# Performance work log

Measured on AMD Instinct MI355X. Metric: run time of the kernel, lower is better.

Reference implementation:

```python
import jax, jax.numpy as jnp
import numpy as np

NUM_PRODUCT = 100000
NUM_USERS = 10000
EMBED_DIM = 512
H = EMBED_DIM // 2          # gru_hidden_size = embedding_dim // 2
MBS = 20                    # max_basket_size
NB = 64                     # baskets per user
K = 256                     # batch of users
B = NB * MBS                # flattened item positions per user
L = 2                       # GRU layers


def setup_inputs() -> dict:
    key = jax.random.key(0)
    ks = jax.random.split(key, 8)
    filter_basket_prob = jax.random.uniform(ks[0], (K, B), dtype=jnp.float32)
    # item ids in [-1, NUM_PRODUCT-1]; -1 is padding (shifted to padding_idx 0)
    input_seq_tensor = jax.random.randint(ks[1], (K, B), 0, NUM_PRODUCT + 1) - 1
    uid = jax.random.randint(ks[2], (K,), 0, NUM_USERS)
    embed_table = 0.02 * jax.random.normal(ks[3], (NUM_PRODUCT + 1, H), dtype=jnp.float32)
    embed_table = embed_table.at[0].set(0.0)  # padding_idx=0
    s = 1.0 / np.sqrt(H)
    w_ih = jax.random.uniform(ks[4], (L, 3 * H, H), jnp.float32, -s, s)
    w_hh = jax.random.uniform(ks[5], (L, 3 * H, H), jnp.float32, -s, s)
    b_ih = jax.random.uniform(ks[6], (L, 3 * H), jnp.float32, -s, s)
    b_hh = jax.random.uniform(ks[7], (L, 3 * H), jnp.float32, -s, s)
    return {"filter_basket_prob": filter_basket_prob, "input_seq_tensor": input_seq_tensor,
            "uid": uid, "embed_table": embed_table,
            "w_ih": w_ih, "w_hh": w_hh, "b_ih": b_ih, "b_hh": b_hh}


def _gru_layer(x, wih, whh, bih, bhh):
    # x: [K, T, H]; torch GRU gate math (r, z, n gate order)
    gi = jnp.einsum('kth,gh->ktg', x, wih) + bih  # [K, T, 3H]

    def step(h, gi_t):
        gh = h @ whh.T + bhh
        ir, iz, inn = jnp.split(gi_t, 3, axis=-1)
        hr, hz, hn = jnp.split(gh, 3, axis=-1)
        r = jax.nn.sigmoid(ir + hr)
        z = jax.nn.sigmoid(iz + hz)
        n = jnp.tanh(inn + r * hn)
        h_new = (1.0 - z) * n + z * h
        return h_new, h_new

    h0 = jnp.zeros((x.shape[0], whh.shape[1]), x.dtype)
    _, hs = jax.lax.scan(step, h0, jnp.swapaxes(gi, 0, 1))  # [T, K, H]
    return jnp.swapaxes(hs, 0, 1)


def reference(filter_basket_prob, input_seq_tensor, uid, embed_table, w_ih, w_hh, b_ih, b_hh):
    Kb, Bb = filter_basket_prob.shape
    Hh = embed_table.shape[1]
    nb = Bb // MBS
    # mask out padding positions (constant w.r.t. grads, as in torch .detach())
    mask = (input_seq_tensor != -1).astype(jnp.float32)
    prob = filter_basket_prob * mask                      # [K, B]
    emb = embed_table[input_seq_tensor + 1]               # [K, B, H]
    emb_f = (emb * prob[..., None]).reshape(Kb, nb, MBS, Hh)
    prob_b = prob.reshape(Kb, nb, MBS)
    filter_b = prob_b.max(axis=-1)                        # [K, NB]
    # avg basket pooling: sum(prob*emb) / (sum(prob) + eps)
    basket_emb = emb_f.sum(axis=2) / (prob_b.sum(axis=-1, keepdims=True) + 1e-10)
    valid = (filter_b > 0).astype(jnp.int32)
    # stable descending sort moves valid baskets to the front, preserving order
    order = jnp.argsort(-valid, axis=-1)                  # [K, NB]
    lengths = valid.sum(axis=-1)
    lengths = lengths + (lengths == 0).astype(lengths.dtype)  # clamp to >= 1
    x = jnp.take_along_axis(basket_emb, order[:, :, None], axis=1)  # [K, NB, H]
    # pack/pad/unsort in the original cancel out: GRU output at t depends only
    # on inputs <= t, so run the full padded scan and read step lengths-1.
    for l in range(w_ih.shape[0]):
        x = _gru_layer(x, w_ih[l], w_hh[l], b_ih[l], b_hh[l])
    return x[jnp.arange(Kb), lengths - 1]                 # [K, H]
```

## Files before the change

### kernel.cpp

```cpp
#include <hip/hip_runtime.h>
#include <cstdint>

#define KU 256
#define NBASK 64
#define MBS 20
#define BITEMS 1280
#define HD 256
#define G3 768
#define TT 64

typedef short v8s __attribute__((ext_vector_type(8)));
typedef float v4f __attribute__((ext_vector_type(4)));
typedef unsigned short v4us __attribute__((ext_vector_type(4)));
typedef unsigned int v4u __attribute__((ext_vector_type(4)));

__device__ __forceinline__ unsigned short f2b(float f){
  uint32_t u = __float_as_uint(f);
  u += 0x7FFFu + ((u >> 16) & 1u);
  return (unsigned short)(u >> 16);
}
__device__ __forceinline__ float b2f(unsigned short s){
  return __uint_as_float(((uint32_t)s) << 16);
}
__device__ __forceinline__ unsigned int packf(float x){
  unsigned short hi = f2b(x);
  unsigned short lo = f2b(x - b2f(hi));
  return ((unsigned int)hi << 16) | lo;
}
__device__ __forceinline__ float unpackf(unsigned int v){
  return b2f((unsigned short)(v >> 16)) + b2f((unsigned short)(v & 0xffffu));
}
__device__ __forceinline__ void waitflag(int* f, int v){
  while (__hip_atomic_load(f, __ATOMIC_ACQUIRE, __HIP_MEMORY_SCOPE_AGENT) < v)
    __builtin_amdgcn_s_sleep(2);
}

__global__ __launch_bounds__(1024) void k_convert(
    const float* __restrict__ wih, const float* __restrict__ whh,
    unsigned short* __restrict__ wih1hi, unsigned short* __restrict__ wih1lo,
    unsigned short* __restrict__ wih2hi, unsigned short* __restrict__ wih2lo,
    unsigned short* __restrict__ whh1hi, unsigned short* __restrict__ whh1lo,
    unsigned short* __restrict__ whh2hi, unsigned short* __restrict__ whh2lo)
{
  int idx = blockIdx.x * 1024 + threadIdx.x;
  int which = blockIdx.y;
  float v;
  if (which == 0)      v = wih[idx];
  else if (which == 1) v = wih[196608 + idx];
  else if (which == 2) v = whh[idx];
  else                 v = whh[196608 + idx];
  unsigned short hi = f2b(v);
  unsigned short lo = f2b(v - b2f(hi));
  if (which == 0)      { wih1hi[idx] = hi; wih1lo[idx] = lo; }
  else if (which == 1) { wih2hi[idx] = hi; wih2lo[idx] = lo; }
  else if (which == 2) { whh1hi[idx] = hi; whh1lo[idx] = lo; }
  else                 { whh2hi[idx] = hi; whh2lo[idx] = lo; }
}

__global__ void k_zero(int* flags){
  if (threadIdx.x < 96) flags[threadIdx.x] = 0;
}

__global__ __launch_bounds__(64) void k_order(
    const float* __restrict__ prob, const int* __restrict__ seq,
    int* __restrict__ order, int* __restrict__ lengths)
{
  int k = blockIdx.x, j = threadIdx.x;
  int base = k * BITEMS + j * MBS;
  float mx = 0.f;
  #pragma unroll
  for (int m = 0; m < MBS; m++) {
    int it = seq[base + m];
    float p = (it >= 0) ? prob[base + m] : 0.f;
    mx = fmaxf(mx, p);
  }
  bool valid = mx > 0.f;
  unsigned long long bal = __ballot(valid);
  int len = __popcll(bal);
  unsigned long long below = bal & ((1ull << j) - 1ull);
  int pos = valid ? __popcll(below) : (len + (j - __popcll(below)));
  order[k * NBASK + j] = pos;
  if (j == 0) lengths[k] = (len > 0) ? len : 1;
}

__global__ __launch_bounds__(256) void k_basket(
    const float* __restrict__ prob, const int* __restrict__ seq,
    const float* __restrict__ table, const int* __restrict__ order,
    unsigned short* __restrict__ xbhi, unsigned short* __restrict__ xblo)
{
  int j = blockIdx.x, k = blockIdx.y;
  int h = threadIdx.x;
  int base = k * BITEMS + j * MBS;
  float acc = 0.f, sp = 0.f;
  #pragma unroll
  for (int m = 0; m < MBS; m++) {
    int it = seq[base + m];
    if (it >= 0) {
      float p = prob[base + m];
      sp += p;
      acc += p * table[(size_t)(it + 1) * HD + h];
    }
  }
  float val = acc / (sp + 1e-10f);
  int dest = order[k * NBASK + j];
  unsigned short hi = f2b(val);
  size_t o = ((size_t)k * NBASK + dest) * HD + h;
  xbhi[o] = hi;
  xblo[o] = f2b(val - b2f(hi));
}

__global__ __launch_bounds__(256) void k_gemm3(
    const unsigned short* __restrict__ Xhi, const unsigned short* __restrict__ Xlo,
    const unsigned short* __restrict__ Whi, const unsigned short* __restrict__ Wlo,
    const float* __restrict__ bias, float* __restrict__ Y)
{
  int nblk = blockIdx.x;
  int mblk = blockIdx.y;
  int wv = threadIdx.x >> 6;
  int l = threadIdx.x & 63;
  int r = l & 15, g = l >> 4;
  int mbase = mblk * 64 + wv * 16;
  int nbase = nblk * 64;
  v4f acc[4];
  #pragma unroll
  for (int c = 0; c < 4; c++) {
    float bn = bias[nbase + c * 16 + r];
    acc[c] = (v4f){bn, bn, bn, bn};
  }
  const unsigned short* xh = Xhi + (size_t)(mbase + r) * HD;
  const unsigned short* xl = Xlo + (size_t)(mbase + r) * HD;
  #pragma unroll
  for (int k0 = 0; k0 < HD; k0 += 32) {
    v8s ahi = *(const v8s*)(xh + k0 + g * 8);
    v8s alo = *(const v8s*)(xl + k0 + g * 8);
    #pragma unroll
    for (int c = 0; c < 4; c++) {
      size_t wo = (size_t)(nbase + c * 16 + r) * HD + k0 + g * 8;
      v8s bhi = *(const v8s*)(Whi + wo);
      v8s blo = *(const v8s*)(Wlo + wo);
      acc[c] = __builtin_amdgcn_mfma_f32_16x16x32_bf16(ahi, bhi, acc[c], 0, 0, 0);
      acc[c] = __builtin_amdgcn_mfma_f32_16x16x32_bf16(alo, bhi, acc[c], 0, 0, 0);
      acc[c] = __builtin_amdgcn_mfma_f32_16x16x32_bf16(ahi, blo, acc[c], 0, 0, 0);
    }
  }
  #pragma unroll
  for (int c = 0; c < 4; c++) {
    int n = nbase + c * 16 + r;
    int mrow = mbase + g * 4;
    #pragma unroll
    for (int i = 0; i < 4; i++)
      Y[(size_t)(mrow + i) * G3 + n] = acc[c][i];
  }
}

__device__ __forceinline__ void wload_all(
    const unsigned short* __restrict__ w0, const unsigned short* __restrict__ w1,
    const unsigned short* __restrict__ w2, int half4,
    v8s (&cw0)[8], v8s (&cw1)[8], v8s (&cw2)[8])
{
  #pragma unroll
  for (int kk = 0; kk < 8; kk++) {
    int p = (half4 + kk) & 7;
    cw0[kk] = *(const v8s*)(w0 + p * 32);
    cw1[kk] = *(const v8s*)(w1 + p * 32);
    cw2[kk] = *(const v8s*)(w2 + p * 32);
  }
}
template<int K0, int KN>
__device__ __forceinline__ void mfma_run(
    const unsigned short (*h_hi)[256], const unsigned short (*h_lo)[256],
    const unsigned short* __restrict__ nlo_s, int r, int g, int jloc, int half4,
    const v8s (&cw0)[8], const v8s (&cw1)[8], const v8s (&cw2)[8],
    v4f& a0, v4f& a1, v4f& a2)
{
  #pragma unroll
  for (int kk = K0; kk < KN; kk++) {
    int p = (half4 + kk) & 7;
    int slotA = ((p * 4 + g) ^ (r & 7)) * 8;
    v8s ahi = *(const v8s*)&h_hi[r][slotA];
    v8s alo = *(const v8s*)&h_lo[r][slotA];
    v8s nl  = *(const v8s*)&nlo_s[jloc * 256 + slotA];
    a0 = __builtin_amdgcn_mfma_f32_16x16x32_bf16(ahi, cw0[kk], a0, 0, 0, 0);
    a0 = __builtin_amdgcn_mfma_f32_16x16x32_bf16(alo, cw0[kk], a0, 0, 0, 0);
    a1 = __builtin_amdgcn_mfma_f32_16x16x32_bf16(ahi, cw1[kk], a1, 0, 0, 0);
    a1 = __builtin_amdgcn_mfma_f32_16x16x32_bf16(alo, cw1[kk], a1, 0, 0, 0);
    a2 = __builtin_amdgcn_mfma_f32_16x16x32_bf16(ahi, cw2[kk], a2, 0, 0, 0);
    a2 = __builtin_amdgcn_mfma_f32_16x16x32_bf16(alo, cw2[kk], a2, 0, 0, 0);
    a2 = __builtin_amdgcn_mfma_f32_16x16x32_bf16(ahi, nl, a2, 0, 0, 0);
  }
}

__global__ __launch_bounds__(512) __attribute__((amdgpu_waves_per_eu(2, 2)))
void k_pipe(
    const unsigned short* __restrict__ whh1hi, const unsigned short* __restrict__ whh1lo,
    const unsigned short* __restrict__ wih2hi, const unsigned short* __restrict__ wih2lo,
    const unsigned short* __restrict__ whh2hi, const unsigned short* __restrict__ whh2lo,
    float* __restrict__ gi, unsigned int* __restrict__ h1pk, unsigned int* __restrict__ h2x,
    const float* __restrict__ bhh1, const float* __restrict__ bih2,
    const float* __restrict__ bhh2,
    const int* __restrict__ lengths, float* __restrict__ out, int* flags)
{
  __shared__ unsigned short h_hi[16][256], h_lo[16][256];
  __shared__ unsigned short nlo_s[32768];
  int tid = threadIdx.x;
  int l = tid & 63, r = l & 15, g = l >> 4;
  int swv = __builtin_amdgcn_readfirstlane(tid >> 6);
  int bx = blockIdx.x;
  int role = bx >> 5, sub = bx & 31, half = sub >> 4, b = sub & 15;
  int half4 = half * 4;
  int ub = b * 16;
  int jloc = swv * 16 + r, j = half * 128 + jloc;
  int* aflag = flags, *gflag = flags + 32, *bflag = flags + 64;
  int myf = sub, sibf = sub ^ 16;

  const unsigned short* whi_g = (role == 0) ? whh1hi : (role == 1) ? wih2hi : whh2hi;
  const unsigned short* wlo_g = (role == 0) ? whh1lo : (role == 1) ? wih2lo : whh2lo;
  const float* bb_ = (role == 0) ? bhh1 : (role == 1) ? bih2 : bhh2;

  for (int idx = tid; idx < 4096; idx += 512) {
    ((unsigned short*)h_hi)[idx] = 0;
    ((unsigned short*)h_lo)[idx] = 0;
  }
  const unsigned short* wlo_n = wlo_g + 2 * 65536 + half * 128 * 256;
  for (int idx = tid; idx < 32768; idx += 512) {
    int row = idx >> 8, col = idx & 255;
    int slot = (col >> 3) ^ (row & 7);
    nlo_s[row * 256 + slot * 8 + (col & 7)] = wlo_n[idx];
  }
  const unsigned short* w0 = whi_g + (size_t)j * 256 + g * 8;
  const unsigned short* w1 = w0 + 65536;
  const unsigned short* w2 = w0 + 131072;
  float b_r = bb_[j], b_z = bb_[256 + j], b_n = bb_[512 + j];
  int sibbase = (1 - half) * 128;
  int xu = tid >> 5;
  __syncthreads();

  if (role == 0) {
    float hold[4] = {0.f, 0.f, 0.f, 0.f};
    const float* gp[4];
    unsigned int* hq[4];
    #pragma unroll
    for (int i = 0; i < 4; i++) {
      gp[i] = gi + (size_t)(ub + g * 4 + i) * TT * G3 + j;
      hq[i] = h1pk + (size_t)(ub + g * 4 + i) * TT * HD + j;
    }
    for (int t = 0; t < TT; t++) {
      v8s cw0[8], cw1[8], cw2[8];
      wload_all(w0, w1, w2, half4, cw0, cw1, cw2);
      float gir[4], giz[4], gin[4];
      #pragma unroll
      for (int i = 0; i < 4; i++) {
        gir[i] = gp[i][0]; giz[i] = gp[i][256]; gin[i] = gp[i][512];
        gp[i] += G3;
      }
      v4f a0 = {0.f,0.f,0.f,0.f}, a1 = {0.f,0.f,0.f,0.f}, a2 = {0.f,0.f,0.f,0.f};
      mfma_run<0,4>(h_hi, h_lo, nlo_s, r, g, jloc, half4, cw0, cw1, cw2, a0, a1, a2);
      if (t > 0 && tid == 0) waitflag(&aflag[sibf], t);
      __syncthreads();
      if (t > 0) {
        int sj = sibbase + (tid & 31) * 4;
        v4u pk = *(const v4u*)&h1pk[((size_t)(ub + xu) * TT + (t - 1)) * HD + sj];
        int pos = (((sj >> 3) ^ (xu & 7)) << 3) + (sj & 7);
        v4us hv, lv;
        #pragma unroll
        for (int i = 0; i < 4; i++) { hv[i] = (unsigned short)(pk[i] >> 16); lv[i] = (unsigned short)(pk[i] & 0xffffu); }
        *(v4us*)&h_hi[xu][pos] = hv;
        *(v4us*)&h_lo[xu][pos] = lv;
      }
      __syncthreads();
      mfma_run<4,8>(h_hi, h_lo, nlo_s, r, g, jloc, half4, cw0, cw1, cw2, a0, a1, a2);
      #pragma unroll
      for (int i = 0; i < 4; i++) {
        float hr = a0[i] + b_r, hz = a1[i] + b_z, hn = a2[i] + b_n;
        float rr = 1.f / (1.f + __expf(-(gir[i] + hr)));
        float zz = 1.f / (1.f + __expf(-(giz[i] + hz)));
        float e  = __expf(2.f * (gin[i] + rr * hn));
        float nn = 1.f - 2.f / (e + 1.f);
        float hnew = (1.f - zz) * nn + zz * hold[i];
        hold[i] = hnew;
        unsigned short h_  = f2b(hnew);
        unsigned short lo_ = f2b(hnew - b2f(h_));
        int u = g * 4 + i;
        int pos = (((j >> 3) ^ (u & 7)) << 3) + (j & 7);
        h_hi[u][pos] = h_;
        h_lo[u][pos] = lo_;
        hq[i][0] = ((unsigned int)h_ << 16) | lo_;
        hq[i] += HD;
      }
      __syncthreads();
      if (tid == 0) {
        __threadfence();
        __hip_atomic_store(&aflag[myf], t + 1, __ATOMIC_RELEASE, __HIP_MEMORY_SCOPE_AGENT);
      }
    }
  } else if (role == 1) {
    unsigned int* gi_u = (unsigned int*)gi;
    for (int t = 0; t < TT; t++) {
      v8s cw0[8], cw1[8], cw2[8];
      wload_all(w0, w1, w2, half4, cw0, cw1, cw2);
      if (tid == 0) { waitflag(&aflag[b], t + 1); waitflag(&aflag[16 + b], t + 1); }
      __syncthreads();
      {
        int c0 = (tid & 31) * 8;
        const unsigned int* src = &h1pk[((size_t)(ub + xu) * TT + t) * HD + c0];
        #pragma unroll
        for (int hf = 0; hf < 2; hf++) {
          v4u pk = *(const v4u*)(src + hf * 4);
          int sj = c0 + hf * 4;
          int pos = (((sj >> 3) ^ (xu & 7)) << 3) + (sj & 7);
          v4us hv, lv;
          #pragma unroll
          for (int i = 0; i < 4; i++) { hv[i] = (unsigned short)(pk[i] >> 16); lv[i] = (unsigned short)(pk[i] & 0xffffu); }
          *(v4us*)&h_hi[xu][pos] = hv;
          *(v4us*)&h_lo[xu][pos] = lv;
        }
      }
      __syncthreads();
      v4f a0 = {b_r, b_r, b_r, b_r}, a1 = {b_z, b_z, b_z, b_z}, a2 = {b_n, b_n, b_n, b_n};
      mfma_run<0,8>(h_hi, h_lo, nlo_s, r, g, jloc, half4, cw0, cw1, cw2, a0, a1, a2);
      #pragma unroll
      for (int i = 0; i < 4; i++) {
        size_t base = ((size_t)(ub + g * 4 + i) * TT + t) * G3;
        gi_u[base + j]       = packf(a0[i]);
        gi_u[base + 256 + j] = packf(a1[i]);
        gi_u[base + 512 + j] = packf(a2[i]);
      }
      __syncthreads();
      if (tid == 0) {
        __threadfence();
        __hip_atomic_store(&gflag[myf], t + 1, __ATOMIC_RELEASE, __HIP_MEMORY_SCOPE_AGENT);
      }
    }
  } else {
    float hold[4] = {0.f, 0.f, 0.f, 0.f};
    const unsigned int* gq[4];
    int lenr[4];
    #pragma unroll
    for (int i = 0; i < 4; i++) {
      gq[i] = (const unsigned int*)gi + (size_t)(ub + g * 4 + i) * TT * G3 + j;
      lenr[i] = lengths[ub + g * 4 + i];
    }
    for (int t = 0; t < TT; t++) {
      v8s cw0[8], cw1[8], cw2[8];
      wload_all(w0, w1, w2, half4, cw0, cw1, cw2);
      v4f a0 = {0.f,0.f,0.f,0.f}, a1 = {0.f,0.f,0.f,0.f}, a2 = {0.f,0.f,0.f,0.f};
      mfma_run<0,4>(h_hi, h_lo, nlo_s, r, g, jloc, half4, cw0, cw1, cw2, a0, a1, a2);
      if (tid == 0) {
        waitflag(&gflag[myf], t + 1);
        if (t > 0) waitflag(&bflag[sibf], t);
      }
      __syncthreads();
      if (t > 0) {
        int sj = sibbase + (tid & 31) * 4;
        v4u pk = *(const v4u*)&h2x[(size_t)(ub + xu) * HD + sj];
        int pos = (((sj >> 3) ^ (xu & 7)) << 3) + (sj & 7);
        v4us hv, lv;
        #pragma unroll
        for (int i = 0; i < 4; i++) { hv[i] = (unsigned short)(pk[i] >> 16); lv[i] = (unsigned short)(pk[i] & 0xffffu); }
        *(v4us*)&h_hi[xu][pos] = hv;
        *(v4us*)&h_lo[xu][pos] = lv;
      }
      unsigned int vr[4], vz[4], vn[4];
      #pragma unroll
      for (int i = 0; i < 4; i++) {
        vr[i] = gq[i][0]; vz[i] = gq[i][256]; vn[i] = gq[i][512];
        gq[i] += G3;
      }
      __syncthreads();
      mfma_run<4,8>(h_hi, h_lo, nlo_s, r, g, jloc, half4, cw0, cw1, cw2, a0, a1, a2);
      #pragma unroll
      for (int i = 0; i < 4; i++) {
        float hr = a0[i] + b_r, hz = a1[i] + b_z, hn = a2[i] + b_n;
        float rr = 1.f / (1.f + __expf(-(unpackf(vr[i]) + hr)));
        float zz = 1.f / (1.f + __expf(-(unpackf(vz[i]) + hz)));
        float e  = __expf(2.f * (unpackf(vn[i]) + rr * hn));
        float nn = 1.f - 2.f / (e + 1.f);
        float hnew = (1.f - zz) * nn + zz * hold[i];
        hold[i] = hnew;
        unsigned short h_  = f2b(hnew);
        unsigned short lo_ = f2b(hnew - b2f(h_));
        int u = g * 4 + i;
        int pos = (((j >> 3) ^ (u & 7)) << 3) + (j & 7);
        h_hi[u][pos] = h_;
        h_lo[u][pos] = lo_;
        h2x[(size_t)(ub + u) * HD + j] = ((unsigned int)h_ << 16) | lo_;
        if (t == lenr[i] - 1)
          out[(size_t)(ub + u) * HD + j] = hnew;
      }
      __syncthreads();
      if (tid == 0) {
        __threadfence();
        __hip_atomic_store(&bflag[myf], t + 1, __ATOMIC_RELEASE, __HIP_MEMORY_SCOPE_AGENT);
      }
    }
  }
}

extern "C" void kernel_launch(void* const* d_in, const int* in_sizes, int n_in,
                              void* d_out, int out_size, void* d_ws, size_t ws_size,
                              hipStream_t stream) {
  const float* prob  = (const float*)d_in[0];
  const int*   seq   = (const int*)d_in[1];
  const float* table = (const float*)d_in[3];
  const float* wih   = (const float*)d_in[4];
  const float* whh   = (const float*)d_in[5];
  const float* bih   = (const float*)d_in[6];
  const float* bhh   = (const float*)d_in[7];
  float* out = (float*)d_out;

  char* ws = (char*)d_ws;
  float* gi            = (float*)ws;
  unsigned short* xbhi = (unsigned short*)(ws + 50331648);
  unsigned short* xblo = (unsigned short*)(ws + 58720256);
  unsigned int* h1pk   = (unsigned int*)xbhi;
  char* wsw = ws + 67108864;
  const size_t WSZ = 393216;
  unsigned short* wih1hi = (unsigned short*)(wsw + 0 * WSZ);
  unsigned short* wih1lo = (unsigned short*)(wsw + 1 * WSZ);
  unsigned short* wih2hi = (unsigned short*)(wsw + 2 * WSZ);
  unsigned short* wih2lo = (unsigned short*)(wsw + 3 * WSZ);
  unsigned short* whh1hi = (unsigned short*)(wsw + 4 * WSZ);
  unsigned short* whh1lo = (unsigned short*)(wsw + 5 * WSZ);
  unsigned short* whh2hi = (unsigned short*)(wsw + 6 * WSZ);
  unsigned short* whh2lo = (unsigned short*)(wsw + 7 * WSZ);
  int* order   = (int*)(wsw + 8 * WSZ);
  int* lengths = order + KU * NBASK;
  int* flags   = lengths + KU;
  unsigned int* h2x = (unsigned int*)wih1hi;

  k_zero<<<1, 128, 0, stream>>>(flags);
  k_convert<<<dim3(192, 4), 1024, 0, stream>>>(wih, whh,
      wih1hi, wih1lo, wih2hi, wih2lo, whh1hi, whh1lo, whh2hi, whh2lo);
  k_order<<<dim3(KU), 64, 0, stream>>>(prob, seq, order, lengths);
  k_basket<<<dim3(NBASK, KU), 256, 0, stream>>>(prob, seq, table, order, xbhi, xblo);
  k_gemm3<<<dim3(12, 256), 256, 0, stream>>>(xbhi, xblo, wih1hi, wih1lo, bih, gi);
  k_pipe<<<dim3(96), 512, 0, stream>>>(
      whh1hi, whh1lo, wih2hi, wih2lo, whh2hi, whh2lo,
      gi, h1pk, h2x, bhh, bih + G3, bhh + G3, lengths, out, flags);
}
```

Measured before the change: 717.1 us.

## Fold layer-1 input projection into persistent pipeline as a fourth role

Removes the standalone layer-1 input GEMM kernel and adds a new role of 32 blocks inside the persistent pipeline kernel. That role computes the layer-1 input gates per timestep and signals them through new flags, so the recurrence can start while later steps are still being projected. Basket embeddings are now written as packed hi/lo words so the new role can read them like the hidden-state buffers. The grid grows from 96 to 128 blocks and the waves-per-EU attribute is dropped, which changes occupancy and adds more inter-block flag traffic on the critical path.

```diff
diff --git a/kernel.cpp b/kernel.cpp
--- a/kernel.cpp
+++ b/kernel.cpp
@@ -58,7 +58,7 @@
 }
 
 __global__ void k_zero(int* flags){
-  if (threadIdx.x < 96) flags[threadIdx.x] = 0;
+  if (threadIdx.x < 128) flags[threadIdx.x] = 0;
 }
 
 __global__ __launch_bounds__(64) void k_order(
@@ -86,7 +86,7 @@
 __global__ __launch_bounds__(256) void k_basket(
     const float* __restrict__ prob, const int* __restrict__ seq,
     const float* __restrict__ table, const int* __restrict__ order,
-    unsigned short* __restrict__ xbhi, unsigned short* __restrict__ xblo)
+    unsigned int* __restrict__ xb)
 {
   int j = blockIdx.x, k = blockIdx.y;
   int h = threadIdx.x;
@@ -103,54 +103,7 @@
   }
   float val = acc / (sp + 1e-10f);
   int dest = order[k * NBASK + j];
-  unsigned short hi = f2b(val);
-  size_t o = ((size_t)k * NBASK + dest) * HD + h;
-  xbhi[o] = hi;
-  xblo[o] = f2b(val - b2f(hi));
-}
-
-__global__ __launch_bounds__(256) void k_gemm3(
-    const unsigned short* __restrict__ Xhi, const unsigned short* __restrict__ Xlo,
-    const unsigned short* __restrict__ Whi, const unsigned short* __restrict__ Wlo,
-    const float* __restrict__ bias, float* __restrict__ Y)
-{
-  int nblk = blockIdx.x;
-  int mblk = blockIdx.y;
-  int wv = threadIdx.x >> 6;
-  int l = threadIdx.x & 63;
-  int r = l & 15, g = l >> 4;
-  int mbase = mblk * 64 + wv * 16;
-  int nbase = nblk * 64;
-  v4f acc[4];
-  #pragma unroll
-  for (int c = 0; c < 4; c++) {
-    float bn = bias[nbase + c * 16 + r];
-    acc[c] = (v4f){bn, bn, bn, bn};
-  }
-  const unsigned short* xh = Xhi + (size_t)(mbase + r) * HD;
-  const unsigned short* xl = Xlo + (size_t)(mbase + r) * HD;
-  #pragma unroll
-  for (int k0 = 0; k0 < HD; k0 += 32) {
-    v8s ahi = *(const v8s*)(xh + k0 + g * 8);
-    v8s alo = *(const v8s*)(xl + k0 + g * 8);
-    #pragma unroll
-    for (int c = 0; c < 4; c++) {
-      size_t wo = (size_t)(nbase + c * 16 + r) * HD + k0 + g * 8;
-      v8s bhi = *(const v8s*)(Whi + wo);
-      v8s blo = *(const v8s*)(Wlo + wo);
-      acc[c] = __builtin_amdgcn_mfma_f32_16x16x32_bf16(ahi, bhi, acc[c], 0, 0, 0);
-      acc[c] = __builtin_amdgcn_mfma_f32_16x16x32_bf16(alo, bhi, acc[c], 0, 0, 0);
-      acc[c] = __builtin_amdgcn_mfma_f32_16x16x32_bf16(ahi, blo, acc[c], 0, 0, 0);
-    }
-  }
-  #pragma unroll
-  for (int c = 0; c < 4; c++) {
-    int n = nbase + c * 16 + r;
-    int mrow = mbase + g * 4;
-    #pragma unroll
-    for (int i = 0; i < 4; i++)
-      Y[(size_t)(mrow + i) * G3 + n] = acc[c][i];
-  }
+  xb[((size_t)k * NBASK + dest) * HD + h] = packf(val);
 }
 
 __device__ __forceinline__ void wload_all(
@@ -190,14 +143,14 @@
   }
 }
 
-__global__ __launch_bounds__(512) __attribute__((amdgpu_waves_per_eu(2, 2)))
-void k_pipe(
+__global__ __launch_bounds__(512) void k_pipe(
+    const unsigned short* __restrict__ wih1hi, const unsigned short* __restrict__ wih1lo,
     const unsigned short* __restrict__ whh1hi, const unsigned short* __restrict__ whh1lo,
     const unsigned short* __restrict__ wih2hi, const unsigned short* __restrict__ wih2lo,
     const unsigned short* __restrict__ whh2hi, const unsigned short* __restrict__ whh2lo,
-    float* __restrict__ gi, unsigned int* __restrict__ h1pk, unsigned int* __restrict__ h2x,
-    const float* __restrict__ bhh1, const float* __restrict__ bih2,
-    const float* __restrict__ bhh2,
+    float* __restrict__ gi, unsigned int* __restrict__ pk, unsigned int* __restrict__ h2x,
+    const float* __restrict__ bih1, const float* __restrict__ bhh1,
+    const float* __restrict__ bih2, const float* __restrict__ bhh2,
     const int* __restrict__ lengths, float* __restrict__ out, int* flags)
 {
   __shared__ unsigned short h_hi[16][256], h_lo[16][256];
@@ -210,12 +163,15 @@
   int half4 = half * 4;
   int ub = b * 16;
   int jloc = swv * 16 + r, j = half * 128 + jloc;
-  int* aflag = flags, *gflag = flags + 32, *bflag = flags + 64;
+  int* aflag = flags, *gflag = flags + 32, *bflag = flags + 64, *g1flag = flags + 96;
   int myf = sub, sibf = sub ^ 16;
 
-  const unsigned short* whi_g = (role == 0) ? whh1hi : (role == 1) ? wih2hi : whh2hi;
-  const unsigned short* wlo_g = (role == 0) ? whh1lo : (role == 1) ? wih2lo : whh2lo;
-  const float* bb_ = (role == 0) ? bhh1 : (role == 1) ? bih2 : bhh2;
+  const unsigned short* whi_g = (role == 0) ? wih1hi : (role == 1) ? whh1hi
+                              : (role == 2) ? wih2hi : whh2hi;
+  const unsigned short* wlo_g = (role == 0) ? wih1lo : (role == 1) ? whh1lo
+                              : (role == 2) ? wih2lo : whh2lo;
+  const float* bb_ = (role == 0) ? bih1 : (role == 1) ? bhh1
+                   : (role == 2) ? bih2 : bhh2;
 
   for (int idx = tid; idx < 4096; idx += 512) {
     ((unsigned short*)h_hi)[idx] = 0;
@@ -235,23 +191,25 @@
   int xu = tid >> 5;
   __syncthreads();
 
-  if (role == 0) {
+  if (role == 1) {
     float hold[4] = {0.f, 0.f, 0.f, 0.f};
-    const float* gp[4];
+    const unsigned int* gq[4];
     unsigned int* hq[4];
     #pragma unroll
     for (int i = 0; i < 4; i++) {
-      gp[i] = gi + (size_t)(ub + g * 4 + i) * TT * G3 + j;
-      hq[i] = h1pk + (size_t)(ub + g * 4 + i) * TT * HD + j;
+      gq[i] = (const unsigned int*)gi + (size_t)(ub + g * 4 + i) * TT * G3 + j;
+      hq[i] = pk + (size_t)(ub + g * 4 + i) * TT * HD + j;
     }
     for (int t = 0; t < TT; t++) {
       v8s cw0[8], cw1[8], cw2[8];
       wload_all(w0, w1, w2, half4, cw0, cw1, cw2);
-      float gir[4], giz[4], gin[4];
-      #pragma unroll
-      for (int i = 0; i < 4; i++) {
-        gir[i] = gp[i][0]; giz[i] = gp[i][256]; gin[i] = gp[i][512];
-        gp[i] += G3;
+      waitflag(&g1flag[b], t + 1);
+      waitflag(&g1flag[16 + b], t + 1);
+      unsigned int vr[4], vz[4], vn[4];
+      #pragma unroll
+      for (int i = 0; i < 4; i++) {
+        vr[i] = gq[i][0]; vz[i] = gq[i][256]; vn[i] = gq[i][512];
+        gq[i] += G3;
       }
       v4f a0 = {0.f,0.f,0.f,0.f}, a1 = {0.f,0.f,0.f,0.f}, a2 = {0.f,0.f,0.f,0.f};
       mfma_run<0,4>(h_hi, h_lo, nlo_s, r, g, jloc, half4, cw0, cw1, cw2, a0, a1, a2);
@@ -259,11 +217,11 @@
       __syncthreads();
       if (t > 0) {
         int sj = sibbase + (tid & 31) * 4;
-        v4u pk = *(const v4u*)&h1pk[((size_t)(ub + xu) * TT + (t - 1)) * HD + sj];
+        v4u pkv = *(const v4u*)&pk[((size_t)(ub + xu) * TT + (t - 1)) * HD + sj];
         int pos = (((sj >> 3) ^ (xu & 7)) << 3) + (sj & 7);
         v4us hv, lv;
         #pragma unroll
-        for (int i = 0; i < 4; i++) { hv[i] = (unsigned short)(pk[i] >> 16); lv[i] = (unsigned short)(pk[i] & 0xffffu); }
+        for (int i = 0; i < 4; i++) { hv[i] = (unsigned short)(pkv[i] >> 16); lv[i] = (unsigned short)(pkv[i] & 0xffffu); }
         *(v4us*)&h_hi[xu][pos] = hv;
         *(v4us*)&h_lo[xu][pos] = lv;
       }
@@ -272,9 +230,9 @@
       #pragma unroll
       for (int i = 0; i < 4; i++) {
         float hr = a0[i] + b_r, hz = a1[i] + b_z, hn = a2[i] + b_n;
-        float rr = 1.f / (1.f + __expf(-(gir[i] + hr)));
-        float zz = 1.f / (1.f + __expf(-(giz[i] + hz)));
-        float e  = __expf(2.f * (gin[i] + rr * hn));
+        float rr = 1.f / (1.f + __expf(-(unpackf(vr[i]) + hr)));
+        float zz = 1.f / (1.f + __expf(-(unpackf(vz[i]) + hz)));
+        float e  = __expf(2.f * (unpackf(vn[i]) + rr * hn));
         float nn = 1.f - 2.f / (e + 1.f);
         float hnew = (1.f - zz) * nn + zz * hold[i];
         hold[i] = hnew;
@@ -293,45 +251,7 @@
         __hip_atomic_store(&aflag[myf], t + 1, __ATOMIC_RELEASE, __HIP_MEMORY_SCOPE_AGENT);
       }
     }
-  } else if (role == 1) {
-    unsigned int* gi_u = (unsigned int*)gi;
-    for (int t = 0; t < TT; t++) {
-      v8s cw0[8], cw1[8], cw2[8];
-      wload_all(w0, w1, w2, half4, cw0, cw1, cw2);
-      if (tid == 0) { waitflag(&aflag[b], t + 1); waitflag(&aflag[16 + b], t + 1); }
-      __syncthreads();
-      {
-        int c0 = (tid & 31) * 8;
-        const unsigned int* src = &h1pk[((size_t)(ub + xu) * TT + t) * HD + c0];
-        #pragma unroll
-        for (int hf = 0; hf < 2; hf++) {
-          v4u pk = *(const v4u*)(src + hf * 4);
-          int sj = c0 + hf * 4;
-          int pos = (((sj >> 3) ^ (xu & 7)) << 3) + (sj & 7);
-          v4us hv, lv;
-          #pragma unroll
-          for (int i = 0; i < 4; i++) { hv[i] = (unsigned short)(pk[i] >> 16); lv[i] = (unsigned short)(pk[i] & 0xffffu); }
-          *(v4us*)&h_hi[xu][pos] = hv;
-          *(v4us*)&h_lo[xu][pos] = lv;
-        }
-      }
-      __syncthreads();
-      v4f a0 = {b_r, b_r, b_r, b_r}, a1 = {b_z, b_z, b_z, b_z}, a2 = {b_n, b_n, b_n, b_n};
-      mfma_run<0,8>(h_hi, h_lo, nlo_s, r, g, jloc, half4, cw0, cw1, cw2, a0, a1, a2);
-      #pragma unroll
-      for (int i = 0; i < 4; i++) {
-        size_t base = ((size_t)(ub + g * 4 + i) * TT + t) * G3;
-        gi_u[base + j]       = packf(a0[i]);
-        gi_u[base + 256 + j] = packf(a1[i]);
-        gi_u[base + 512 + j] = packf(a2[i]);
-      }
-      __syncthreads();
-      if (tid == 0) {
-        __threadfence();
-        __hip_atomic_store(&gflag[myf], t + 1, __ATOMIC_RELEASE, __HIP_MEMORY_SCOPE_AGENT);
-      }
-    }
-  } else {
+  } else if (role == 3) {
     float hold[4] = {0.f, 0.f, 0.f, 0.f};
     const unsigned int* gq[4];
     int lenr[4];
@@ -352,11 +272,11 @@
       __syncthreads();
       if (t > 0) {
         int sj = sibbase + (tid & 31) * 4;
-        v4u pk = *(const v4u*)&h2x[(size_t)(ub + xu) * HD + sj];
+        v4u pkv = *(const v4u*)&h2x[(size_t)(ub + xu) * HD + sj];
         int pos = (((sj >> 3) ^ (xu & 7)) << 3) + (sj & 7);
         v4us hv, lv;
         #pragma unroll
-        for (int i = 0; i < 4; i++) { hv[i] = (unsigned short)(pk[i] >> 16); lv[i] = (unsigned short)(pk[i] & 0xffffu); }
+        for (int i = 0; i < 4; i++) { hv[i] = (unsigned short)(pkv[i] >> 16); lv[i] = (unsigned short)(pkv[i] & 0xffffu); }
         *(v4us*)&h_hi[xu][pos] = hv;
         *(v4us*)&h_lo[xu][pos] = lv;
       }
@@ -393,6 +313,45 @@
         __hip_atomic_store(&bflag[myf], t + 1, __ATOMIC_RELEASE, __HIP_MEMORY_SCOPE_AGENT);
       }
     }
+  } else {
+    unsigned int* gi_u = (unsigned int*)gi;
+    int* postf = (role == 0) ? &g1flag[myf] : &gflag[myf];
+    for (int t = 0; t < TT; t++) {
+      v8s cw0[8], cw1[8], cw2[8];
+      wload_all(w0, w1, w2, half4, cw0, cw1, cw2);
+      if (role == 2 && tid == 0) { waitflag(&aflag[b], t + 1); waitflag(&aflag[16 + b], t + 1); }
+      __syncthreads();
+      {
+        int c0 = (tid & 31) * 8;
+        const unsigned int* src = &pk[((size_t)(ub + xu) * TT + t) * HD + c0];
+        #pragma unroll
+        for (int hf = 0; hf < 2; hf++) {
+          v4u pkv = *(const v4u*)(src + hf * 4);
+          int sj = c0 + hf * 4;
+          int pos = (((sj >> 3) ^ (xu & 7)) << 3) + (sj & 7);
+          v4us hv, lv;
+          #pragma unroll
+          for (int i = 0; i < 4; i++) { hv[i] = (unsigned short)(pkv[i] >> 16); lv[i] = (unsigned short)(pkv[i] & 0xffffu); }
+          *(v4us*)&h_hi[xu][pos] = hv;
+          *(v4us*)&h_lo[xu][pos] = lv;
+        }
+      }
+      __syncthreads();
+      v4f a0 = {b_r, b_r, b_r, b_r}, a1 = {b_z, b_z, b_z, b_z}, a2 = {b_n, b_n, b_n, b_n};
+      mfma_run<0,8>(h_hi, h_lo, nlo_s, r, g, jloc, half4, cw0, cw1, cw2, a0, a1, a2);
+      #pragma unroll
+      for (int i = 0; i < 4; i++) {
+        size_t base = ((size_t)(ub + g * 4 + i) * TT + t) * G3;
+        gi_u[base + j]       = packf(a0[i]);
+        gi_u[base + 256 + j] = packf(a1[i]);
+        gi_u[base + 512 + j] = packf(a2[i]);
+      }
+      __syncthreads();
+      if (tid == 0) {
+        __threadfence();
+        __hip_atomic_store(postf, t + 1, __ATOMIC_RELEASE, __HIP_MEMORY_SCOPE_AGENT);
+      }
+    }
   }
 }
 
@@ -409,10 +368,8 @@
   float* out = (float*)d_out;
 
   char* ws = (char*)d_ws;
-  float* gi            = (float*)ws;
-  unsigned short* xbhi = (unsigned short*)(ws + 50331648);
-  unsigned short* xblo = (unsigned short*)(ws + 58720256);
-  unsigned int* h1pk   = (unsigned int*)xbhi;
+  float* gi          = (float*)ws;
+  unsigned int* pk   = (unsigned int*)(ws + 50331648);
   char* wsw = ws + 67108864;
   const size_t WSZ = 393216;
   unsigned short* wih1hi = (unsigned short*)(wsw + 0 * WSZ);
@@ -426,15 +383,14 @@
   int* order   = (int*)(wsw + 8 * WSZ);
   int* lengths = order + KU * NBASK;
   int* flags   = lengths + KU;
-  unsigned int* h2x = (unsigned int*)wih1hi;
+  unsigned int* h2x = (unsigned int*)(wsw + 8 * WSZ + 131072);
 
   k_zero<<<1, 128, 0, stream>>>(flags);
   k_convert<<<dim3(192, 4), 1024, 0, stream>>>(wih, whh,
       wih1hi, wih1lo, wih2hi, wih2lo, whh1hi, whh1lo, whh2hi, whh2lo);
   k_order<<<dim3(KU), 64, 0, stream>>>(prob, seq, order, lengths);
-  k_basket<<<dim3(NBASK, KU), 256, 0, stream>>>(prob, seq, table, order, xbhi, xblo);
-  k_gemm3<<<dim3(12, 256), 256, 0, stream>>>(xbhi, xblo, wih1hi, wih1lo, bih, gi);
-  k_pipe<<<dim3(96), 512, 0, stream>>>(
-      whh1hi, whh1lo, wih2hi, wih2lo, whh2hi, whh2lo,
-      gi, h1pk, h2x, bhh, bih + G3, bhh + G3, lengths, out, flags);
-}
+  k_basket<<<dim3(NBASK, KU), 256, 0, stream>>>(prob, seq, table, order, pk);
+  k_pipe<<<dim3(128), 512, 0, stream>>>(
+      wih1hi, wih1lo, whh1hi, whh1lo, wih2hi, wih2lo, whh2hi, whh2lo,
+      gi, pk, h2x, bih, bhh, bih + G3, bhh + G3, lengths, out, flags);
+}
```

New measurement: 1.228 ms. 1.71x slower.
